# Optimization experiments

Hardware: AMD Instinct MI355X
Metric: run time of the kernel (lower is better)

The kernel has to match this reference:

```python
import jax, jax.numpy as jnp
import numpy as np

EPS = 1e-6
NEG_SLOPE = 0.2


def knn_idx(xf, k):
    # xf: (B, C, N) flattened vector features; returns (B, N, k) neighbor indices
    xx = jnp.sum(xf * xf, axis=1)                       # (B, N)
    inner = jnp.einsum('bcn,bcm->bnm', xf, xf)          # (B, N, N)
    neg_dist = 2.0 * inner - xx[:, :, None] - xx[:, None, :]  # -||xi-xj||^2
    _, idx = jax.lax.top_k(neg_dist, k)                 # includes self (dist 0)
    return idx


def get_graph_feature(x, k):
    # x: (B, D, 3, N) -> edge features (B, 2D, 3, N, k)
    B, D, _, N = x.shape
    idx = knn_idx(x.reshape(B, D * 3, N), k)            # (B, N, k)
    pts = jnp.transpose(x, (0, 3, 1, 2))                # (B, N, D, 3)
    neigh = jax.vmap(lambda p, i: p[i])(pts, idx)       # (B, N, k, D, 3) gather
    center = jnp.broadcast_to(pts[:, :, None], neigh.shape)
    feat = jnp.concatenate([neigh - center, center], axis=3)  # (B, N, k, 2D, 3)
    return jnp.transpose(feat, (0, 3, 4, 1, 2))


def vn_linear_leakyrelu(x, Wf, Wd):
    # Vector-Neuron linear + leaky ReLU. x: (B, Cin, 3, ...),
    # Wf: (Cout, Cin), Wd: (Cout, Cin) or (1, Cin) when nonlinearity is shared.
    p = jnp.einsum('oi,bi...->bo...', Wf, x)
    d = jnp.einsum('oi,bi...->bo...', Wd, x)
    dot = jnp.sum(p * d, axis=2, keepdims=True)
    dsq = jnp.sum(d * d, axis=2, keepdims=True)
    proj = p - (dot / (dsq + EPS)) * d
    return NEG_SLOPE * p + (1.0 - NEG_SLOPE) * jnp.where(dot >= 0, p, proj)


def setup_inputs() -> dict:
    key = jax.random.key(0)
    ks = jax.random.split(key, 11)
    B, N = 8, 1024
    x = jax.random.normal(ks[0], (B, 3, N), dtype=jnp.float32)
    # dims = [1, 21, 21, 42, 85, 341]
    ins = [2, 42, 42, 84, 169]      # 2*dim_in for edge layers; sum(dims[1:-1]) for last
    outs = [21, 21, 42, 85, 341]
    dirs = [21, 21, 42, 85, 1]      # last layer has share_nonlinearity=True
    d = {"x": x}
    for i, (ci, co, cd) in enumerate(zip(ins, outs, dirs)):
        s = 1.0 / np.sqrt(ci)
        kf, kd = jax.random.split(ks[1 + i])
        d[f"Wf{i}"] = (jax.random.normal(kf, (co, ci), dtype=jnp.float32) * s)
        d[f"Wd{i}"] = (jax.random.normal(kd, (cd, ci), dtype=jnp.float32) * s)
    d["k"] = 20
    return d


def reference(x, Wf0, Wd0, Wf1, Wd1, Wf2, Wd2, Wf3, Wd3, Wf4, Wd4, k):
    cur = x[:, None]                 # (B, 1, 3, N)
    feats = []
    for Wf, Wd in ((Wf0, Wd0), (Wf1, Wd1), (Wf2, Wd2), (Wf3, Wd3)):
        g = get_graph_feature(cur, k)        # (B, 2D, 3, N, k)
        h = vn_linear_leakyrelu(g, Wf, Wd)   # (B, Dout, 3, N, k)
        cur = h.mean(axis=-1)                # mean over neighbors -> (B, Dout, 3, N)
        feats.append(cur)
    xcat = jnp.concatenate(feats, axis=1)    # (B, 169, 3, N)
    out = vn_linear_leakyrelu(xcat, Wf4, Wd4)
    return out.mean(axis=-1)                 # mean over points -> (B, 341, 3)
```

## Files before the change

kernel.cpp:

```cpp
#include <hip/hip_runtime.h>
#include <cstddef>

#define BB 8
#define NN 1024
#define KK 20
#define CCAT 169
#define NT 16

__global__ __launch_bounds__(256) void dist_tile_kernel(
    const float* __restrict__ src, int bs, int F, float* __restrict__ dist) {
  __shared__ float As[8][128];
  __shared__ float Bs[8][128];
  int b = blockIdx.z;
  int rem = blockIdx.x, bi = 0;
  while (rem >= 8 - bi) { rem -= 8 - bi; ++bi; }
  int bj = bi + rem;
  int n0 = bi * 128;
  int m0 = bj * 128;
  int t = threadIdx.x;
  int tx = t & 15, ty = t >> 4;
  const float* p = src + (size_t)b * bs;

  float acc[8][8];
  float xn[8], xm[8];
#pragma unroll
  for (int i = 0; i < 8; ++i) {
    xn[i] = 0.f;
    xm[i] = 0.f;
#pragma unroll
    for (int j = 0; j < 8; ++j) acc[i][j] = 0.f;
  }

  int fr = t >> 5;
  int cc = (t & 31) << 2;
  for (int f0 = 0; f0 < F; f0 += 8) {
    int f = f0 + fr;
    float4 av = {0.f, 0.f, 0.f, 0.f}, bv = {0.f, 0.f, 0.f, 0.f};
    if (f < F) {
      av = *(const float4*)(p + (size_t)f * NN + n0 + cc);
      bv = *(const float4*)(p + (size_t)f * NN + m0 + cc);
    }
    __syncthreads();
    *(float4*)&As[fr][cc] = av;
    *(float4*)&Bs[fr][cc] = bv;
    __syncthreads();
#pragma unroll
    for (int f2 = 0; f2 < 8; ++f2) {
      float4 al = *(const float4*)&As[f2][ty << 2];
      float4 ah = *(const float4*)&As[f2][64 + (ty << 2)];
      float4 bl = *(const float4*)&Bs[f2][tx << 2];
      float4 bh = *(const float4*)&Bs[f2][64 + (tx << 2)];
      float a[8] = {al.x, al.y, al.z, al.w, ah.x, ah.y, ah.z, ah.w};
      float bb[8] = {bl.x, bl.y, bl.z, bl.w, bh.x, bh.y, bh.z, bh.w};
#pragma unroll
      for (int i = 0; i < 8; ++i) xn[i] += a[i] * a[i];
#pragma unroll
      for (int j = 0; j < 8; ++j) xm[j] += bb[j] * bb[j];
#pragma unroll
      for (int i = 0; i < 8; ++i)
#pragma unroll
        for (int j = 0; j < 8; ++j) acc[i][j] += a[i] * bb[j];
    }
  }

#pragma unroll
  for (int i = 0; i < 8; ++i)
#pragma unroll
    for (int j = 0; j < 8; ++j) acc[i][j] = 2.f * acc[i][j] - xn[i] - xm[j];

#pragma unroll
  for (int i = 0; i < 8; ++i) {
    int n = n0 + ((i < 4) ? ((ty << 2) + i) : (64 + (ty << 2) + i - 4));
    float* dr = dist + (((size_t)b * NN + n) << 10);
    *(float4*)(dr + m0 + (tx << 2)) =
        make_float4(acc[i][0], acc[i][1], acc[i][2], acc[i][3]);
    *(float4*)(dr + m0 + 64 + (tx << 2)) =
        make_float4(acc[i][4], acc[i][5], acc[i][6], acc[i][7]);
  }

  if (bi != bj) {
#pragma unroll
    for (int j = 0; j < 8; ++j) {
      int m = m0 + ((j < 4) ? ((tx << 2) + j) : (64 + (tx << 2) + j - 4));
      float* dr = dist + (((size_t)b * NN + m) << 10);
      *(float4*)(dr + n0 + (ty << 2)) =
          make_float4(acc[0][j], acc[1][j], acc[2][j], acc[3][j]);
      *(float4*)(dr + n0 + 64 + (ty << 2)) =
          make_float4(acc[4][j], acc[5][j], acc[6][j], acc[7][j]);
    }
  }
}

__device__ __forceinline__ unsigned long long shfl_xor_u64(
    unsigned long long v, int off) {
  unsigned lo = (unsigned)v, hi = (unsigned)(v >> 32);
  lo = __shfl_xor(lo, off, 64);
  hi = __shfl_xor(hi, off, 64);
  return ((unsigned long long)hi << 32) | lo;
}

__global__ __launch_bounds__(256) void topk_kernel(
    const float* __restrict__ dist, int* __restrict__ idx_out) {
  int wave = threadIdx.x >> 6;
  int lane = threadIdx.x & 63;
  int row = blockIdx.x * 4 + wave;
  const float* d = dist + ((size_t)row << 10);

  unsigned long long key[16];
#pragma unroll
  for (int s = 0; s < 16; ++s) {
    int m = lane + (s << 6);
    unsigned u = __float_as_uint(d[m]);
    u = (u & 0x80000000u) ? ~u : (u | 0x80000000u);
    key[s] = ((unsigned long long)u << 32) | (unsigned)(NN - 1 - m);
  }

#pragma unroll
  for (int size = 2; size <= 16; size <<= 1) {
#pragma unroll
    for (int stride = size >> 1; stride > 0; stride >>= 1) {
#pragma unroll
      for (int i = 0; i < 16; ++i) {
        int j = i ^ stride;
        if (j > i) {
          unsigned long long a = key[i], c = key[j];
          bool desc = ((i & size) == 0);
          bool sw = desc ? (a < c) : (a > c);
          key[i] = sw ? c : a;
          key[j] = sw ? a : c;
        }
      }
    }
  }

  int* out = idx_out + row * KK;
  unsigned long long head = key[0];
  for (int r = 0; r < KK; ++r) {
    unsigned long long w = head;
#pragma unroll
    for (int off = 32; off > 0; off >>= 1) {
      unsigned long long o = shfl_xor_u64(w, off);
      if (o > w) w = o;
    }
    if (lane == 0) out[r] = (NN - 1) - (int)(w & 0xFFFFFFFFull);
    if (head == w) {
#pragma unroll
      for (int s = 0; s < 15; ++s) key[s] = key[s + 1];
      key[15] = 0ull;
      head = key[0];
    }
  }
}

template <int DD>
__global__ __launch_bounds__(256) void edge_fused_kernel(
    const float* __restrict__ src, int bs, int Co, int nsplit,
    const float* __restrict__ Wf, const float* __restrict__ Wd,
    const int* __restrict__ idx, int ooff, float* __restrict__ xcat) {
  __shared__ float2 Ulds[3 * NN];
  __shared__ float2 Vlds[3 * NN];
  __shared__ float4 Wlds[48];
  int bo = blockIdx.x;
  int b = bo / Co, o = bo % Co;
  int t = threadIdx.x;

  if (t < DD) {
    float wfa = Wf[o * 2 * DD + t];
    float wfb = Wf[o * 2 * DD + DD + t] - wfa;
    float wda = Wd[o * 2 * DD + t];
    float wdb = Wd[o * 2 * DD + DD + t] - wda;
    Wlds[t] = make_float4(wfa, wfb, wda, wdb);
  }
  __syncthreads();

  const float* sb = src + (size_t)b * bs;
  {
    int c0 = t << 2;
    float4 uf[3], vf[3], ud[3], vd[3];
#pragma unroll
    for (int r = 0; r < 3; ++r) {
      uf[r] = make_float4(0.f, 0.f, 0.f, 0.f);
      vf[r] = make_float4(0.f, 0.f, 0.f, 0.f);
      ud[r] = make_float4(0.f, 0.f, 0.f, 0.f);
      vd[r] = make_float4(0.f, 0.f, 0.f, 0.f);
    }
#pragma unroll 2
    for (int i = 0; i < DD; ++i) {
      const float* row = sb + (size_t)i * 3 * NN + c0;
      float4 s[3];
      s[0] = *(const float4*)(row);
      s[1] = *(const float4*)(row + 1024);
      s[2] = *(const float4*)(row + 2048);
      float4 w = Wlds[i];
#pragma unroll
      for (int r = 0; r < 3; ++r) {
        uf[r].x += w.x * s[r].x; uf[r].y += w.x * s[r].y;
        uf[r].z += w.x * s[r].z; uf[r].w += w.x * s[r].w;
        vf[r].x += w.y * s[r].x; vf[r].y += w.y * s[r].y;
        vf[r].z += w.y * s[r].z; vf[r].w += w.y * s[r].w;
        ud[r].x += w.z * s[r].x; ud[r].y += w.z * s[r].y;
        ud[r].z += w.z * s[r].z; ud[r].w += w.z * s[r].w;
        vd[r].x += w.w * s[r].x; vd[r].y += w.w * s[r].y;
        vd[r].z += w.w * s[r].z; vd[r].w += w.w * s[r].w;
      }
    }
#pragma unroll
    for (int r = 0; r < 3; ++r) {
      int g = t + 256 * r;
      *(float4*)&Ulds[(g << 2) + 0] =
          make_float4(uf[r].x, ud[r].x, uf[r].y, ud[r].y);
      *(float4*)&Ulds[(g << 2) + 2] =
          make_float4(uf[r].z, ud[r].z, uf[r].w, ud[r].w);
      *(float4*)&Vlds[(g << 2) + 0] =
          make_float4(vf[r].x, vd[r].x, vf[r].y, vd[r].y);
      *(float4*)&Vlds[(g << 2) + 2] =
          make_float4(vf[r].z, vd[r].z, vf[r].w, vd[r].w);
    }
  }
  __syncthreads();

  const float inv_k = 1.f / KK;
  int cnt = NN / nsplit;
  int nbase = blockIdx.y * cnt;
  for (int n = nbase + t; n < nbase + cnt; n += 256) {
    float2 v0 = Vlds[n];
    float2 v1 = Vlds[NN + n];
    float2 v2 = Vlds[2 * NN + n];
    const int4* ip = (const int4*)(idx + (b * NN + n) * KK);
    float a0 = 0.f, a1 = 0.f, a2 = 0.f;
#pragma unroll
    for (int q = 0; q < 5; ++q) {
      int4 iv = ip[q];
      int nbs[4] = {iv.x, iv.y, iv.z, iv.w};
#pragma unroll
      for (int jj = 0; jj < 4; ++jj) {
        int nb = nbs[jj];
        float2 u0 = Ulds[nb];
        float2 u1 = Ulds[NN + nb];
        float2 u2 = Ulds[2 * NN + nb];
        float pf0 = u0.x + v0.x, pd0 = u0.y + v0.y;
        float pf1 = u1.x + v1.x, pd1 = u1.y + v1.y;
        float pf2 = u2.x + v2.x, pd2 = u2.y + v2.y;
        float dot = pf0 * pd0 + pf1 * pd1 + pf2 * pd2;
        float dsq = pd0 * pd0 + pd1 * pd1 + pd2 * pd2;
        float g = (dot >= 0.f) ? 0.f : 0.8f * dot / (dsq + 1e-6f);
        a0 += pf0 - g * pd0;
        a1 += pf1 - g * pd1;
        a2 += pf2 - g * pd2;
      }
    }
    size_t ob = (size_t)b * CCAT * 3 * NN + (size_t)(ooff + o) * 3 * NN + n;
    xcat[ob] = a0 * inv_k;
    xcat[ob + NN] = a1 * inv_k;
    xcat[ob + 2 * NN] = a2 * inv_k;
  }
}

__global__ __launch_bounds__(256) void final_fused_kernel(
    const float* __restrict__ xcat, const float* __restrict__ Wf4,
    const float* __restrict__ Wd4, float* __restrict__ part) {
  __shared__ float Ws[16][64];
  __shared__ float Xs[3][16][64];
  __shared__ float Wds[16];
  int b = blockIdx.z;
  int o0 = blockIdx.y * 64;
  int n0 = blockIdx.x * 64;
  int t = threadIdx.x;
  int tx = t & 15, ty = t >> 4;

  float acc[3][4][4];
  float dv[3][4];
#pragma unroll
  for (int c = 0; c < 3; ++c) {
#pragma unroll
    for (int i = 0; i < 4; ++i)
#pragma unroll
      for (int j = 0; j < 4; ++j) acc[c][i][j] = 0.f;
#pragma unroll
    for (int j = 0; j < 4; ++j) dv[c][j] = 0.f;
  }

  const float* xb = xcat + (size_t)b * CCAT * 3 * NN;
  for (int f0 = 0; f0 < CCAT; f0 += 16) {
    int f = f0 + ty;
    float4 xv[3];
#pragma unroll
    for (int c = 0; c < 3; ++c) {
      xv[c] = make_float4(0.f, 0.f, 0.f, 0.f);
      if (f < CCAT)
        xv[c] = *(const float4*)(xb + ((size_t)f * 3 + c) * NN + n0 + (tx << 2));
    }
    float wv[4];
#pragma unroll
    for (int q = 0; q < 4; ++q) {
      int o = o0 + (tx << 2) + q;
      wv[q] = (o < 341 && f < CCAT) ? Wf4[o * CCAT + f] : 0.f;
    }
    float wdv = 0.f;
    if (t < 16 && f0 + t < CCAT) wdv = Wd4[f0 + t];
    __syncthreads();
#pragma unroll
    for (int c = 0; c < 3; ++c) *(float4*)&Xs[c][ty][tx << 2] = xv[c];
    *(float4*)&Ws[ty][tx << 2] = make_float4(wv[0], wv[1], wv[2], wv[3]);
    if (t < 16) Wds[t] = wdv;
    __syncthreads();
#pragma unroll
    for (int f2 = 0; f2 < 16; ++f2) {
      float4 w = *(const float4*)&Ws[f2][ty << 2];
      float wa[4] = {w.x, w.y, w.z, w.w};
      float wd = Wds[f2];
#pragma unroll
      for (int c = 0; c < 3; ++c) {
        float4 x = *(const float4*)&Xs[c][f2][tx << 2];
        float xa[4] = {x.x, x.y, x.z, x.w};
#pragma unroll
        for (int j = 0; j < 4; ++j) dv[c][j] += wd * xa[j];
#pragma unroll
        for (int i = 0; i < 4; ++i)
#pragma unroll
          for (int j = 0; j < 4; ++j) acc[c][i][j] += wa[i] * xa[j];
      }
    }
  }

  float s[3][4];
#pragma unroll
  for (int c = 0; c < 3; ++c)
#pragma unroll
    for (int i = 0; i < 4; ++i) s[c][i] = 0.f;
#pragma unroll
  for (int i = 0; i < 4; ++i) {
#pragma unroll
    for (int j = 0; j < 4; ++j) {
      float d0 = dv[0][j], d1 = dv[1][j], d2 = dv[2][j];
      float p0 = acc[0][i][j], p1 = acc[1][i][j], p2 = acc[2][i][j];
      float dot = p0 * d0 + p1 * d1 + p2 * d2;
      float dsq = d0 * d0 + d1 * d1 + d2 * d2;
      float g = (dot >= 0.f) ? 0.f : 0.8f * dot / (dsq + 1e-6f);
      s[0][i] += p0 - g * d0;
      s[1][i] += p1 - g * d1;
      s[2][i] += p2 - g * d2;
    }
  }

#pragma unroll
  for (int off = 1; off < 16; off <<= 1) {
#pragma unroll
    for (int c = 0; c < 3; ++c)
#pragma unroll
      for (int i = 0; i < 4; ++i) s[c][i] += __shfl_xor(s[c][i], off, 64);
  }
  if (tx == 0) {
#pragma unroll
    for (int i = 0; i < 4; ++i) {
      int o = o0 + (ty << 2) + i;
      if (o < 341) {
#pragma unroll
        for (int c = 0; c < 3; ++c)
          part[(((size_t)b * 341 + o) * 3 + c) * NT + blockIdx.x] = s[c][i];
      }
    }
  }
}

__global__ void final_reduce_kernel(const float* __restrict__ part,
                                    float* __restrict__ out) {
  int t = blockIdx.x * 256 + threadIdx.x;
  if (t >= BB * 341 * 3) return;
  const float* p = part + (size_t)t * NT;
  float s = 0.f;
#pragma unroll
  for (int nt = 0; nt < NT; ++nt) s += p[nt];
  out[t] = s * (1.f / 1024.f);
}

extern "C" void kernel_launch(void* const* d_in, const int* in_sizes, int n_in,
                              void* d_out, int out_size, void* d_ws,
                              size_t ws_size, hipStream_t stream) {
  (void)in_sizes; (void)n_in; (void)out_size; (void)ws_size;
  const float* x = (const float*)d_in[0];
  const float* Wf[5] = {(const float*)d_in[1], (const float*)d_in[3],
                        (const float*)d_in[5], (const float*)d_in[7],
                        (const float*)d_in[9]};
  const float* Wd[5] = {(const float*)d_in[2], (const float*)d_in[4],
                        (const float*)d_in[6], (const float*)d_in[8],
                        (const float*)d_in[10]};

  float* ws = (float*)d_ws;
  float* dist = ws;
  float* part = ws;
  size_t off = (size_t)BB * NN * NN;
  int* idx = (int*)(ws + off);
  off += (size_t)BB * NN * KK;
  float* xcat = ws + off;

  struct LayerCfg { int D, Co, inoff, ooff, nsplit; };
  const LayerCfg L[4] = {
      {1, 21, 0, 0, 4},
      {21, 21, 0, 21, 4},
      {21, 42, 21, 42, 2},
      {42, 85, 42, 84, 1},
  };

  for (int l = 0; l < 4; ++l) {
    const float* src = (l == 0) ? x : (xcat + (size_t)L[l].inoff * 3 * NN);
    int bs = (l == 0) ? 3 * NN : CCAT * 3 * NN;
    int D = L[l].D, Co = L[l].Co;

    dist_tile_kernel<<<dim3(36, 1, BB), 256, 0, stream>>>(src, bs, 3 * D, dist);
    topk_kernel<<<(BB * NN) / 4, 256, 0, stream>>>(dist, idx);
    dim3 eg(BB * Co, L[l].nsplit);
    if (D == 1)
      edge_fused_kernel<1><<<eg, 256, 0, stream>>>(
          src, bs, Co, L[l].nsplit, Wf[l], Wd[l], idx, L[l].ooff, xcat);
    else if (D == 21)
      edge_fused_kernel<21><<<eg, 256, 0, stream>>>(
          src, bs, Co, L[l].nsplit, Wf[l], Wd[l], idx, L[l].ooff, xcat);
    else
      edge_fused_kernel<42><<<eg, 256, 0, stream>>>(
          src, bs, Co, L[l].nsplit, Wf[l], Wd[l], idx, L[l].ooff, xcat);
  }

  final_fused_kernel<<<dim3(NT, 6, BB), 256, 0, stream>>>(xcat, Wf[4], Wd[4],
                                                          part);
  final_reduce_kernel<<<(BB * 341 * 3 + 255) / 256, 256, 0, stream>>>(
      part, (float*)d_out);
}
```

Before: 428.7 us.

## Double-buffer final GEMM tiles and precompute shared direction vector separately

The final fused kernel now double-buffers its shared-memory tiles, prefetching the next feature tile into registers while computing the current one, which halves the barriers per tile. The shared-direction dot product against Wd4 moves out of the fused kernel into a small dvec_kernel that writes per-point direction vectors to workspace; the fused kernel reads them before the nonlinearity. This removes redundant direction accumulation across the 6 output-channel blocks but adds a launch and an extra pass over xcat. The final stage is a small part of the total runtime.

```diff
diff --git a/kernel.cpp b/kernel.cpp
--- a/kernel.cpp
+++ b/kernel.cpp
@@ -256,12 +256,24 @@
   }
 }
 
+__global__ __launch_bounds__(256) void dvec_kernel(
+    const float* __restrict__ xcat, const float* __restrict__ Wd4,
+    float* __restrict__ dvg) {
+  int t = blockIdx.x * 256 + threadIdx.x;
+  int b = t >> 11;
+  b = t / 3072;
+  int r = t - b * 3072;
+  const float* xp = xcat + (size_t)b * CCAT * 3 * NN + r;
+  float s = 0.f;
+  for (int f = 0; f < CCAT; ++f) s += Wd4[f] * xp[(size_t)f * 3 * NN];
+  dvg[t] = s;
+}
+
 __global__ __launch_bounds__(256) void final_fused_kernel(
     const float* __restrict__ xcat, const float* __restrict__ Wf4,
-    const float* __restrict__ Wd4, float* __restrict__ part) {
-  __shared__ float Ws[16][64];
-  __shared__ float Xs[3][16][64];
-  __shared__ float Wds[16];
+    const float* __restrict__ dvg, float* __restrict__ part) {
+  __shared__ float Ws[2][16][64];
+  __shared__ float Xs[2][3][16][64];
   int b = blockIdx.z;
   int o0 = blockIdx.y * 64;
   int n0 = blockIdx.x * 64;
@@ -269,58 +281,80 @@
   int tx = t & 15, ty = t >> 4;
 
   float acc[3][4][4];
-  float dv[3][4];
-#pragma unroll
-  for (int c = 0; c < 3; ++c) {
+#pragma unroll
+  for (int c = 0; c < 3; ++c)
 #pragma unroll
     for (int i = 0; i < 4; ++i)
 #pragma unroll
       for (int j = 0; j < 4; ++j) acc[c][i][j] = 0.f;
-#pragma unroll
-    for (int j = 0; j < 4; ++j) dv[c][j] = 0.f;
-  }
 
   const float* xb = xcat + (size_t)b * CCAT * 3 * NN;
-  for (int f0 = 0; f0 < CCAT; f0 += 16) {
-    int f = f0 + ty;
-    float4 xv[3];
-#pragma unroll
-    for (int c = 0; c < 3; ++c) {
-      xv[c] = make_float4(0.f, 0.f, 0.f, 0.f);
-      if (f < CCAT)
-        xv[c] = *(const float4*)(xb + ((size_t)f * 3 + c) * NN + n0 + (tx << 2));
-    }
-    float wv[4];
+  const int NTILE = (CCAT + 15) / 16;
+
+  float4 xv[3];
+  float wv[4];
+  {
+    int f = ty;
+#pragma unroll
+    for (int c = 0; c < 3; ++c)
+      xv[c] = *(const float4*)(xb + ((size_t)f * 3 + c) * NN + n0 + (tx << 2));
 #pragma unroll
     for (int q = 0; q < 4; ++q) {
       int o = o0 + (tx << 2) + q;
-      wv[q] = (o < 341 && f < CCAT) ? Wf4[o * CCAT + f] : 0.f;
-    }
-    float wdv = 0.f;
-    if (t < 16 && f0 + t < CCAT) wdv = Wd4[f0 + t];
+      wv[q] = (o < 341) ? Wf4[(size_t)o * CCAT + f] : 0.f;
+    }
+#pragma unroll
+    for (int c = 0; c < 3; ++c) *(float4*)&Xs[0][c][ty][tx << 2] = xv[c];
+    *(float4*)&Ws[0][ty][tx << 2] = make_float4(wv[0], wv[1], wv[2], wv[3]);
+  }
+
+#pragma unroll 1
+  for (int tt = 0; tt < NTILE; ++tt) {
+    int buf = tt & 1;
     __syncthreads();
-#pragma unroll
-    for (int c = 0; c < 3; ++c) *(float4*)&Xs[c][ty][tx << 2] = xv[c];
-    *(float4*)&Ws[ty][tx << 2] = make_float4(wv[0], wv[1], wv[2], wv[3]);
-    if (t < 16) Wds[t] = wdv;
-    __syncthreads();
+    if (tt + 1 < NTILE) {
+      int f = (tt + 1) * 16 + ty;
+#pragma unroll
+      for (int c = 0; c < 3; ++c) {
+        xv[c] = make_float4(0.f, 0.f, 0.f, 0.f);
+        if (f < CCAT)
+          xv[c] =
+              *(const float4*)(xb + ((size_t)f * 3 + c) * NN + n0 + (tx << 2));
+      }
+#pragma unroll
+      for (int q = 0; q < 4; ++q) {
+        int o = o0 + (tx << 2) + q;
+        wv[q] = (o < 341 && f < CCAT) ? Wf4[(size_t)o * CCAT + f] : 0.f;
+      }
+    }
 #pragma unroll
     for (int f2 = 0; f2 < 16; ++f2) {
-      float4 w = *(const float4*)&Ws[f2][ty << 2];
+      float4 w = *(const float4*)&Ws[buf][f2][ty << 2];
       float wa[4] = {w.x, w.y, w.z, w.w};
-      float wd = Wds[f2];
 #pragma unroll
       for (int c = 0; c < 3; ++c) {
-        float4 x = *(const float4*)&Xs[c][f2][tx << 2];
+        float4 x = *(const float4*)&Xs[buf][c][f2][tx << 2];
         float xa[4] = {x.x, x.y, x.z, x.w};
 #pragma unroll
-        for (int j = 0; j < 4; ++j) dv[c][j] += wd * xa[j];
-#pragma unroll
         for (int i = 0; i < 4; ++i)
 #pragma unroll
           for (int j = 0; j < 4; ++j) acc[c][i][j] += wa[i] * xa[j];
       }
     }
+    if (tt + 1 < NTILE) {
+#pragma unroll
+      for (int c = 0; c < 3; ++c) *(float4*)&Xs[buf ^ 1][c][ty][tx << 2] = xv[c];
+      *(float4*)&Ws[buf ^ 1][ty][tx << 2] =
+          make_float4(wv[0], wv[1], wv[2], wv[3]);
+    }
+  }
+
+  float dvv[3][4];
+#pragma unroll
+  for (int c = 0; c < 3; ++c) {
+    float4 dq = *(const float4*)(dvg + (size_t)b * 3 * NN + c * NN + n0 +
+                                 (tx << 2));
+    dvv[c][0] = dq.x; dvv[c][1] = dq.y; dvv[c][2] = dq.z; dvv[c][3] = dq.w;
   }
 
   float s[3][4];
@@ -332,7 +366,7 @@
   for (int i = 0; i < 4; ++i) {
 #pragma unroll
     for (int j = 0; j < 4; ++j) {
-      float d0 = dv[0][j], d1 = dv[1][j], d2 = dv[2][j];
+      float d0 = dvv[0][j], d1 = dvv[1][j], d2 = dvv[2][j];
       float p0 = acc[0][i][j], p1 = acc[1][i][j], p2 = acc[2][i][j];
       float dot = p0 * d0 + p1 * d1 + p2 * d2;
       float dsq = d0 * d0 + d1 * d1 + d2 * d2;
@@ -389,6 +423,7 @@
   float* ws = (float*)d_ws;
   float* dist = ws;
   float* part = ws;
+  float* dvg = ws + (1 << 22);
   size_t off = (size_t)BB * NN * NN;
   int* idx = (int*)(ws + off);
   off += (size_t)BB * NN * KK;
@@ -421,7 +456,8 @@
           src, bs, Co, L[l].nsplit, Wf[l], Wd[l], idx, L[l].ooff, xcat);
   }
 
-  final_fused_kernel<<<dim3(NT, 6, BB), 256, 0, stream>>>(xcat, Wf[4], Wd[4],
+  dvec_kernel<<<(BB * 3 * NN) / 256, 256, 0, stream>>>(xcat, Wd[4], dvg);
+  final_fused_kernel<<<dim3(NT, 6, BB), 256, 0, stream>>>(xcat, Wf[4], dvg,
                                                           part);
   final_reduce_kernel<<<(BB * 341 * 3 + 255) / 256, 256, 0, stream>>>(
       part, (float*)d_out);
```

After: 464.9 us. +8.4%, slower.

## Double-buffer final GEMM tiles via direct global-to-LDS loads with pre-transposed weights

Applied to the files above, without the earlier changes.

Adds a prep kernel that transposes and zero-pads Wf4 into a workspace buffer. The final fused kernel then streams weight and xcat tiles straight into LDS with global_load_lds, using two buffers so the next tile loads while the current one computes. Wd4 is preloaded into LDS once. This is meant to hide global load latency and remove the strided, uncoalesced weight reads, at the cost of an extra kernel launch and more LDS.

```diff
diff --git a/kernel.cpp b/kernel.cpp
--- a/kernel.cpp
+++ b/kernel.cpp
@@ -6,6 +6,7 @@
 #define KK 20
 #define CCAT 169
 #define NT 16
+#define WTLD 384
 
 __global__ __launch_bounds__(256) void dist_tile_kernel(
     const float* __restrict__ src, int bs, int F, float* __restrict__ dist) {
@@ -256,18 +257,37 @@
   }
 }
 
+__global__ __launch_bounds__(256) void prep_kernel(
+    const float* __restrict__ Wf4, float* __restrict__ Wt,
+    float* __restrict__ zpad) {
+  int o = blockIdx.x * 256 + threadIdx.x;
+  int f = blockIdx.y;
+  if (o < WTLD)
+    Wt[(size_t)f * WTLD + o] = (f < CCAT && o < 341) ? Wf4[o * CCAT + f] : 0.f;
+  if (blockIdx.x == 0 && blockIdx.y == 0) zpad[threadIdx.x] = 0.f;
+}
+
+__device__ __forceinline__ void gl2lds16(const float* g, float* l) {
+  __builtin_amdgcn_global_load_lds(
+      (const __attribute__((address_space(1))) unsigned int*)g,
+      (__attribute__((address_space(3))) unsigned int*)l, 16, 0, 0);
+}
+
 __global__ __launch_bounds__(256) void final_fused_kernel(
-    const float* __restrict__ xcat, const float* __restrict__ Wf4,
-    const float* __restrict__ Wd4, float* __restrict__ part) {
-  __shared__ float Ws[16][64];
-  __shared__ float Xs[3][16][64];
-  __shared__ float Wds[16];
+    const float* __restrict__ xcat, const float* __restrict__ Wt,
+    const float* __restrict__ Wd4, const float* __restrict__ zpad,
+    float* __restrict__ part) {
+  __shared__ float Ws[2][16][64];
+  __shared__ float Xs[2][3][16][64];
+  __shared__ float Wda[176];
   int b = blockIdx.z;
   int o0 = blockIdx.y * 64;
   int n0 = blockIdx.x * 64;
   int t = threadIdx.x;
   int tx = t & 15, ty = t >> 4;
 
+  if (t < 176) Wda[t] = (t < CCAT) ? Wd4[t] : 0.f;
+
   float acc[3][4][4];
   float dv[3][4];
 #pragma unroll
@@ -281,37 +301,42 @@
   }
 
   const float* xb = xcat + (size_t)b * CCAT * 3 * NN;
-  for (int f0 = 0; f0 < CCAT; f0 += 16) {
-    int f = f0 + ty;
-    float4 xv[3];
+  const int NTILE = 11;
+
+  {
+    const float* wsrc = Wt + (size_t)ty * WTLD + o0 + (tx << 2);
+    gl2lds16(wsrc, &Ws[0][ty][tx << 2]);
 #pragma unroll
     for (int c = 0; c < 3; ++c) {
-      xv[c] = make_float4(0.f, 0.f, 0.f, 0.f);
-      if (f < CCAT)
-        xv[c] = *(const float4*)(xb + ((size_t)f * 3 + c) * NN + n0 + (tx << 2));
-    }
-    float wv[4];
-#pragma unroll
-    for (int q = 0; q < 4; ++q) {
-      int o = o0 + (tx << 2) + q;
-      wv[q] = (o < 341 && f < CCAT) ? Wf4[o * CCAT + f] : 0.f;
-    }
-    float wdv = 0.f;
-    if (t < 16 && f0 + t < CCAT) wdv = Wd4[f0 + t];
+      const float* xsrc = xb + ((size_t)ty * 3 + c) * NN + n0 + (tx << 2);
+      gl2lds16(xsrc, &Xs[0][c][ty][tx << 2]);
+    }
+  }
+
+#pragma unroll 1
+  for (int tt = 0; tt < NTILE; ++tt) {
+    int buf = tt & 1;
     __syncthreads();
-#pragma unroll
-    for (int c = 0; c < 3; ++c) *(float4*)&Xs[c][ty][tx << 2] = xv[c];
-    *(float4*)&Ws[ty][tx << 2] = make_float4(wv[0], wv[1], wv[2], wv[3]);
-    if (t < 16) Wds[t] = wdv;
-    __syncthreads();
+    if (tt + 1 < NTILE) {
+      int f = (tt + 1) * 16 + ty;
+      const float* wsrc = Wt + (size_t)f * WTLD + o0 + (tx << 2);
+      gl2lds16(wsrc, &Ws[buf ^ 1][ty][tx << 2]);
+#pragma unroll
+      for (int c = 0; c < 3; ++c) {
+        const float* xsrc = (f < CCAT)
+                                ? xb + ((size_t)f * 3 + c) * NN + n0 + (tx << 2)
+                                : zpad + (tx << 2);
+        gl2lds16(xsrc, &Xs[buf ^ 1][c][ty][tx << 2]);
+      }
+    }
 #pragma unroll
     for (int f2 = 0; f2 < 16; ++f2) {
-      float4 w = *(const float4*)&Ws[f2][ty << 2];
+      float4 w = *(const float4*)&Ws[buf][f2][ty << 2];
       float wa[4] = {w.x, w.y, w.z, w.w};
-      float wd = Wds[f2];
+      float wd = Wda[tt * 16 + f2];
 #pragma unroll
       for (int c = 0; c < 3; ++c) {
-        float4 x = *(const float4*)&Xs[c][f2][tx << 2];
+        float4 x = *(const float4*)&Xs[buf][c][f2][tx << 2];
         float xa[4] = {x.x, x.y, x.z, x.w};
 #pragma unroll
         for (int j = 0; j < 4; ++j) dv[c][j] += wd * xa[j];
@@ -389,6 +414,8 @@
   float* ws = (float*)d_ws;
   float* dist = ws;
   float* part = ws;
+  float* Wt = ws + 262144;
+  float* zpad = Wt + 176 * WTLD;
   size_t off = (size_t)BB * NN * NN;
   int* idx = (int*)(ws + off);
   off += (size_t)BB * NN * KK;
@@ -421,8 +448,9 @@
           src, bs, Co, L[l].nsplit, Wf[l], Wd[l], idx, L[l].ooff, xcat);
   }
 
-  final_fused_kernel<<<dim3(NT, 6, BB), 256, 0, stream>>>(xcat, Wf[4], Wd[4],
-                                                          part);
+  prep_kernel<<<dim3(2, 176), 256, 0, stream>>>(Wf[4], Wt, zpad);
+  final_fused_kernel<<<dim3(NT, 6, BB), 256, 0, stream>>>(xcat, Wt, Wd[4],
+                                                          zpad, part);
   final_reduce_kernel<<<(BB * 341 * 3 + 255) / 256, 256, 0, stream>>>(
       part, (float*)d_out);
 }
```

Result: no change. 427.0 us (-0.4%).
